# Optimization experiments

Hardware: AMD Instinct MI355X
Metric: run time of the kernel (lower is better)

## Reference

```python
import jax, jax.numpy as jnp
import numpy as np

V, E, D, B = 8192, 48, 64, 256  # nodes, hyperedges, feat dim, graphs (32 nodes/graph)


def setup_inputs() -> dict:
    key = jax.random.key(0)
    k1, k2, k3, k4 = jax.random.split(key, 4)
    x = jax.random.normal(k1, (V, D), dtype=jnp.float32)
    H = (jax.random.uniform(k2, (V, E)) < 0.3).astype(jnp.float32)
    W = jax.random.normal(k3, (D, D), dtype=jnp.float32) / np.sqrt(D)
    b = jax.random.normal(k4, (D,), dtype=jnp.float32) * 0.01
    # equal-sized graphs: node i belongs to graph i // (V//B)
    batch = jnp.repeat(jnp.arange(B, dtype=jnp.int32), V // B)
    return {"x": x, "H": H, "W": W, "b": b, "batch": batch, "num_graphs": B}


def reference(x, H, W, b, batch, num_graphs):
    Vn, Dd = x.shape
    Ee = H.shape[1]
    # edge_emb_tensor = x.unsqueeze(1) * H.unsqueeze(2)  -> (V, E, d)
    edge_emb = x[:, None, :] * H[:, :, None]
    # scatter mean over nodes by graph id -> (B, E, d)
    counts = jax.ops.segment_sum(jnp.ones((Vn,), x.dtype), batch, num_segments=num_graphs)
    sums = jax.ops.segment_sum(edge_emb.reshape(Vn, Ee * Dd), batch, num_segments=num_graphs)
    edge_dim = (sums / counts[:, None]).reshape(num_graphs, Ee, Dd)
    # MLP f: Linear(d,d) + ReLU (torch Linear: x @ W.T + b)
    edge_dim = jax.nn.relu(jnp.einsum('bed,fd->bef', edge_dim, W) + b)
    # repeat_interleave by per-graph node counts == gather by batch index -> (V, E, d)
    node_emb = (edge_dim[batch] * H[:, :, None]).mean(axis=1)  # (V, d)
    h_e = edge_dim.reshape(num_graphs * Ee, Dd)
    # global mean pool over nodes per graph -> (B, d)
    c = jax.ops.segment_sum(node_emb, batch, num_segments=num_graphs) / counts[:, None]
    return c, h_e
```

## Files before the change

### kernel.cpp

```cpp
#include <hip/hip_runtime.h>

constexpr int V   = 8192;
constexpr int E   = 48;
constexpr int D   = 64;
constexpr int B   = 256;
constexpr int NPG = 32;

__global__ __launch_bounds__(256) void hgnn_kernel(
    const float* __restrict__ x,
    const float* __restrict__ Hm,
    const float* __restrict__ W,
    const float* __restrict__ b,
    float* __restrict__ out_c,
    float* __restrict__ out_he)
{
    __shared__ float x_lds[NPG][D];
    __shared__ float H_lds[NPG][E];
    __shared__ float Wt[D][D + 1];
    __shared__ float M_lds[E][D];
    __shared__ float Hbar[E];
    __shared__ float b_lds[D];
    __shared__ float cpart[4][D];

    const int g    = blockIdx.x;
    const int t    = threadIdx.x;
    const int lane = t & 63;
    const int wave = t >> 6;

    const float4* x4  = reinterpret_cast<const float4*>(x + (size_t)g * NPG * D);
    float4*       xl4 = reinterpret_cast<float4*>(&x_lds[0][0]);
    xl4[t]       = x4[t];
    xl4[t + 256] = x4[t + 256];

    const float4* h4  = reinterpret_cast<const float4*>(Hm + (size_t)g * NPG * E);
    float4*       hl4 = reinterpret_cast<float4*>(&H_lds[0][0]);
    hl4[t] = h4[t];
    if (t < 128) hl4[256 + t] = h4[256 + t];

    for (int i = t; i < D * D; i += 256) {
        int f = i >> 6, d = i & 63;
        Wt[d][f] = W[i];
    }
    if (t < D) b_lds[t] = b[t];
    __syncthreads();

    if (t < E) {
        float s = 0.f;
        #pragma unroll
        for (int v = 0; v < NPG; ++v) s += H_lds[v][t];
        Hbar[t] = s * (1.f / NPG);
    }

    float acc[12];
    #pragma unroll
    for (int i = 0; i < 12; ++i) acc[i] = 0.f;
    for (int v = 0; v < NPG; ++v) {
        float xv = x_lds[v][lane];
        #pragma unroll
        for (int i = 0; i < 12; ++i)
            acc[i] += H_lds[v][wave + i * 4] * xv;
    }
    #pragma unroll
    for (int i = 0; i < 12; ++i)
        M_lds[wave + i * 4][lane] = acc[i] * (1.f / NPG);
    __syncthreads();

    float y[12];
    #pragma unroll
    for (int i = 0; i < 12; ++i) y[i] = 0.f;
    for (int d = 0; d < D; ++d) {
        float wv = Wt[d][lane];
        #pragma unroll
        for (int i = 0; i < 12; ++i)
            y[i] += M_lds[wave + i * 4][d] * wv;
    }
    float bb   = b_lds[lane];
    float csum = 0.f;
    #pragma unroll
    for (int i = 0; i < 12; ++i) {
        int   e = wave + i * 4;
        float v = y[i] + bb;
        v = v > 0.f ? v : 0.f;
        out_he[((size_t)g * E + e) * D + lane] = v;
        csum += v * Hbar[e];
    }
    cpart[wave][lane] = csum;
    __syncthreads();

    if (wave == 0) {
        float c = (cpart[0][lane] + cpart[1][lane] + cpart[2][lane] + cpart[3][lane]) * (1.f / E);
        out_c[(size_t)g * D + lane] = c;
    }
}

extern "C" void kernel_launch(void* const* d_in, const int* in_sizes, int n_in,
                              void* d_out, int out_size, void* d_ws, size_t ws_size,
                              hipStream_t stream) {
    (void)in_sizes; (void)n_in; (void)d_ws; (void)ws_size; (void)out_size;
    const float* x  = (const float*)d_in[0];
    const float* Hm = (const float*)d_in[1];
    const float* W  = (const float*)d_in[2];
    const float* b  = (const float*)d_in[3];
    float* out    = (float*)d_out;
    float* out_c  = out;
    float* out_he = out + B * D;
    hgnn_kernel<<<B, 256, 0, stream>>>(x, Hm, W, b, out_c, out_he);
}
```

Baseline: 14.20 us.

## Apply W to node features first, keep W in registers, use 512 threads

Reorders the computation as H^T (x W^T) rather than (H^T x) W^T. Each thread now holds one row of W in registers, which removes the transposed W tile from shared memory and the strided transpose loads. A transposed H copy is built in LDS so H and P can be read as float4, and Hbar is folded into the second contraction. The block size doubles to 8 waves. In exchange the kernel uses 64 extra float registers per thread, which may lower occupancy.

```diff
diff --git a/kernel.cpp b/kernel.cpp
--- a/kernel.cpp
+++ b/kernel.cpp
@@ -5,8 +5,11 @@
 constexpr int D   = 64;
 constexpr int B   = 256;
 constexpr int NPG = 32;
+constexpr int THREADS = 512, WAVES = 8;
+constexpr int EPW = E / WAVES;
+constexpr int RPW = NPG / WAVES;
 
-__global__ __launch_bounds__(256) void hgnn_kernel(
+__global__ __launch_bounds__(THREADS) void hgnn_kernel(
     const float* __restrict__ x,
     const float* __restrict__ Hm,
     const float* __restrict__ W,
@@ -15,81 +18,87 @@
     float* __restrict__ out_he)
 {
     __shared__ float x_lds[NPG][D];
-    __shared__ float H_lds[NPG][E];
-    __shared__ float Wt[D][D + 1];
-    __shared__ float M_lds[E][D];
-    __shared__ float Hbar[E];
-    __shared__ float b_lds[D];
-    __shared__ float cpart[4][D];
+    __shared__ float H_lin[NPG * E];
+    __shared__ float Ht[E][NPG];
+    __shared__ float P_lds[NPG][D];
+    __shared__ float cpart[WAVES][D];
 
     const int g    = blockIdx.x;
     const int t    = threadIdx.x;
     const int lane = t & 63;
     const int wave = t >> 6;
 
-    const float4* x4  = reinterpret_cast<const float4*>(x + (size_t)g * NPG * D);
-    float4*       xl4 = reinterpret_cast<float4*>(&x_lds[0][0]);
-    xl4[t]       = x4[t];
-    xl4[t + 256] = x4[t + 256];
+    float4 wreg[16];
+    const float4* Wrow = reinterpret_cast<const float4*>(W + (size_t)lane * D);
+    #pragma unroll
+    for (int k = 0; k < 16; ++k) wreg[k] = Wrow[k];
 
-    const float4* h4  = reinterpret_cast<const float4*>(Hm + (size_t)g * NPG * E);
-    float4*       hl4 = reinterpret_cast<float4*>(&H_lds[0][0]);
-    hl4[t] = h4[t];
-    if (t < 128) hl4[256 + t] = h4[256 + t];
-
-    for (int i = t; i < D * D; i += 256) {
-        int f = i >> 6, d = i & 63;
-        Wt[d][f] = W[i];
-    }
-    if (t < D) b_lds[t] = b[t];
+    reinterpret_cast<float4*>(&x_lds[0][0])[t] =
+        reinterpret_cast<const float4*>(x + (size_t)g * NPG * D)[t];
+    if (t < 384)
+        reinterpret_cast<float4*>(H_lin)[t] =
+            reinterpret_cast<const float4*>(Hm + (size_t)g * NPG * E)[t];
+    const float bb = b[lane];
     __syncthreads();
 
-    if (t < E) {
-        float s = 0.f;
-        #pragma unroll
-        for (int v = 0; v < NPG; ++v) s += H_lds[v][t];
-        Hbar[t] = s * (1.f / NPG);
+    #pragma unroll
+    for (int k = 0; k < 3; ++k) {
+        int j = t + k * THREADS;
+        int e = j >> 5, v = j & 31;
+        Ht[e][v] = H_lin[v * E + e];
     }
 
-    float acc[12];
-    #pragma unroll
-    for (int i = 0; i < 12; ++i) acc[i] = 0.f;
-    for (int v = 0; v < NPG; ++v) {
-        float xv = x_lds[v][lane];
+    {
+        float acc[RPW] = {0.f, 0.f, 0.f, 0.f};
         #pragma unroll
-        for (int i = 0; i < 12; ++i)
-            acc[i] += H_lds[v][wave + i * 4] * xv;
+        for (int k = 0; k < 16; ++k) {
+            const float4 w4 = wreg[k];
+            #pragma unroll
+            for (int r = 0; r < RPW; ++r) {
+                const float4 x4 =
+                    reinterpret_cast<const float4*>(&x_lds[wave * RPW + r][0])[k];
+                acc[r] += x4.x * w4.x + x4.y * w4.y + x4.z * w4.z + x4.w * w4.w;
+            }
+        }
+        #pragma unroll
+        for (int r = 0; r < RPW; ++r)
+            P_lds[wave * RPW + r][lane] = acc[r];
     }
-    #pragma unroll
-    for (int i = 0; i < 12; ++i)
-        M_lds[wave + i * 4][lane] = acc[i] * (1.f / NPG);
     __syncthreads();
 
-    float y[12];
+    float y[EPW], hs[EPW];
     #pragma unroll
-    for (int i = 0; i < 12; ++i) y[i] = 0.f;
-    for (int d = 0; d < D; ++d) {
-        float wv = Wt[d][lane];
+    for (int i = 0; i < EPW; ++i) { y[i] = 0.f; hs[i] = 0.f; }
+    const int e0 = wave * EPW;
+    #pragma unroll
+    for (int k = 0; k < NPG / 4; ++k) {
+        float4 p4;
+        p4.x = P_lds[4 * k + 0][lane];
+        p4.y = P_lds[4 * k + 1][lane];
+        p4.z = P_lds[4 * k + 2][lane];
+        p4.w = P_lds[4 * k + 3][lane];
         #pragma unroll
-        for (int i = 0; i < 12; ++i)
-            y[i] += M_lds[wave + i * 4][d] * wv;
+        for (int i = 0; i < EPW; ++i) {
+            const float4 h4 = reinterpret_cast<const float4*>(&Ht[e0 + i][0])[k];
+            y[i]  += h4.x * p4.x + h4.y * p4.y + h4.z * p4.z + h4.w * p4.w;
+            hs[i] += (h4.x + h4.y) + (h4.z + h4.w);
+        }
     }
-    float bb   = b_lds[lane];
     float csum = 0.f;
     #pragma unroll
-    for (int i = 0; i < 12; ++i) {
-        int   e = wave + i * 4;
-        float v = y[i] + bb;
-        v = v > 0.f ? v : 0.f;
-        out_he[((size_t)g * E + e) * D + lane] = v;
-        csum += v * Hbar[e];
+    for (int i = 0; i < EPW; ++i) {
+        float yv = fmaxf(y[i] * (1.f / NPG) + bb, 0.f);
+        out_he[((size_t)g * E + e0 + i) * D + lane] = yv;
+        csum += yv * hs[i];
     }
     cpart[wave][lane] = csum;
     __syncthreads();
 
-    if (wave == 0) {
-        float c = (cpart[0][lane] + cpart[1][lane] + cpart[2][lane] + cpart[3][lane]) * (1.f / E);
-        out_c[(size_t)g * D + lane] = c;
+    if (t < D) {
+        float c = 0.f;
+        #pragma unroll
+        for (int w = 0; w < WAVES; ++w) c += cpart[w][t];
+        out_c[(size_t)g * D + t] = c * (1.f / (NPG * E));
     }
 }
 
@@ -104,5 +113,5 @@
     float* out    = (float*)d_out;
     float* out_c  = out;
     float* out_he = out + B * D;
-    hgnn_kernel<<<B, 256, 0, stream>>>(x, Hm, W, b, out_c, out_he);
+    hgnn_kernel<<<B, THREADS, 0, stream>>>(x, Hm, W, b, out_c, out_he);
 }
```

New measurement: 14.68 us. 1.03x slower.
